# Kernel optimization log

Measured on AMD Instinct MI355X. Metric: run time of the kernel, lower is better.

## Reference

```python
import jax, jax.numpy as jnp
import numpy as np

H, HKV, D, HID = 64, 8, 64, 2880
T = 2048
WINDOW = 128
THETA = 150000.0
FACTOR = 32.0
ORIG_MAX = 4096
BETA_FAST, BETA_SLOW = 32.0, 1.0
EPS = 1e-5
SCALE = D ** -0.5
MSCALE = float(0.1 * np.log(FACTOR) + 1.0)  # vLLM YaRN attention mscale


def _yarn_inv_freq():
    # vLLM YaRNScalingRotaryEmbedding inverse frequencies
    def corr_dim(n_rot):
        return D * np.log(ORIG_MAX / (n_rot * 2.0 * np.pi)) / (2.0 * np.log(THETA))
    low = max(int(np.floor(corr_dim(BETA_FAST))), 0)
    high = min(int(np.ceil(corr_dim(BETA_SLOW))), D - 1)
    pow_ = np.arange(0, D, 2, dtype=np.float32) / D
    extrap = 1.0 / (THETA ** pow_)                 # extrapolation inv_freq
    interp = extrap / FACTOR                        # interpolation inv_freq
    ramp = np.clip((np.arange(D // 2, dtype=np.float32) - low) / max(high - low, 1e-3), 0.0, 1.0)
    extrap_mask = 1.0 - ramp
    inv_freq = interp * (1.0 - extrap_mask) + extrap * extrap_mask
    return jnp.asarray(inv_freq, jnp.float32)

_INV_FREQ = _yarn_inv_freq()


def _rope(positions, x):
    # neox-style rotation; x: [T, heads, D]
    freqs = positions.astype(jnp.float32)[:, None] * _INV_FREQ[None, :]  # [T, D/2]
    cos = (jnp.cos(freqs) * MSCALE)[:, None, :]
    sin = (jnp.sin(freqs) * MSCALE)[:, None, :]
    x1, x2 = x[..., : D // 2], x[..., D // 2 :]
    return jnp.concatenate([x1 * cos - x2 * sin, x2 * cos + x1 * sin], axis=-1)


def _attn(q, k, v, sinks):
    # q: [T,H,D]; k,v: [T,HKV,D]; sinks: [H] extra softmax logit per head
    g = H // HKV
    k = jnp.repeat(k, g, axis=1)
    v = jnp.repeat(v, g, axis=1)
    scores = jnp.einsum('qhd,khd->hqk', q, k) * SCALE  # [H,T,T]
    i = jnp.arange(T)[:, None]
    j = jnp.arange(T)[None, :]
    mask = (j <= i) & (i - j < WINDOW)  # causal + sliding window (even layer)
    scores = jnp.where(mask[None], scores, -jnp.inf)
    s = sinks[:, None]                                    # [H,1]
    m = jnp.maximum(jnp.max(scores, axis=-1), s)          # [H,T]
    p = jnp.exp(scores - m[..., None])                    # [H,T,T]
    denom = jnp.sum(p, axis=-1) + jnp.exp(s - m)          # sink adds to denominator only
    out = jnp.einsum('hqk,khd->qhd', p, v) / denom.T[..., None]
    return out.reshape(T, H * D)


def setup_inputs() -> dict:
    key = jax.random.key(0)
    ks = jax.random.split(key, 8)
    return {
        'hidden_states': jax.random.normal(ks[0], (T, HID), jnp.float32),
        'positions': jnp.arange(T, dtype=jnp.int32),
        'norm_w': jnp.ones((HID,), jnp.float32),
        'w_qkv': jax.random.normal(ks[1], ((H + 2 * HKV) * D, HID), jnp.float32) * 0.02,
        'b_qkv': jax.random.normal(ks[2], ((H + 2 * HKV) * D,), jnp.float32) * 0.02,
        'w_o': jax.random.normal(ks[3], (HID, H * D), jnp.float32) * 0.02,
        'b_o': jax.random.normal(ks[4], (HID,), jnp.float32) * 0.02,
        'sinks': jax.random.normal(ks[5], (H,), jnp.float32),
    }


def reference(hidden_states, positions, norm_w, w_qkv, b_qkv, w_o, b_o, sinks):
    x = hidden_states
    t = x * jax.lax.rsqrt(jnp.mean(x * x, axis=-1, keepdims=True) + EPS) * norm_w  # RMSNorm
    qkv = t @ w_qkv.T + b_qkv
    q, k, v = jnp.split(qkv, [H * D, H * D + HKV * D], axis=-1)
    q = _rope(positions, q.reshape(T, H, D))
    k = _rope(positions, k.reshape(T, HKV, D))
    v = v.reshape(T, HKV, D)
    attn_out = _attn(q, k, v, sinks)
    out = attn_out @ w_o.T + b_o
    return out + x  # residual
```

## Files before the change

### kernel.cpp

```cpp
#include <hip/hip_runtime.h>
#include <hip/hip_bf16.h>
#include <stdint.h>

typedef __attribute__((ext_vector_type(8))) short bf16x8;
typedef __attribute__((ext_vector_type(4))) float f32x4;
typedef __attribute__((ext_vector_type(4))) unsigned short u16x4;

#define T_SEQ 2048
#define HID_D 2880
#define KPAD 2944
#define NH 64
#define NKV 8
#define HD 64
#define QKV_N 5120
#define ATT_N 4096
#define WIN 128
#define RSCALE 0.125f
#define MSCALE 1.3465735903f
#define ROPE_TOT (T_SEQ * (NH + NKV) * 32)
#define VT_TOT (NKV * HD * T_SEQ)

__device__ __forceinline__ unsigned short f2bf(float f) {
  union { float f; unsigned u; } v; v.f = f;
  unsigned r = v.u + 0x7fffu + ((v.u >> 16) & 1u);
  return (unsigned short)(r >> 16);
}
__device__ __forceinline__ float bf2f(unsigned short u) {
  union { unsigned u; float f; } v; v.u = ((unsigned)u) << 16;
  return v.f;
}

__device__ __forceinline__ void gload_lds16(const void* g, void* l) {
  __builtin_amdgcn_global_load_lds((const __attribute__((address_space(1))) char*)g,
                                   (__attribute__((address_space(3))) char*)l, 16, 0, 0);
}

__global__ __launch_bounds__(256) void pre_kernel(const float* __restrict__ x,
                                                  const float* __restrict__ w,
                                                  unsigned short* __restrict__ t_bf,
                                                  const float* __restrict__ wq_src,
                                                  unsigned short* __restrict__ wq_dst) {
  __shared__ float red[256];
  if (blockIdx.x < 2048) {
    int row = blockIdx.x;
    const float4* xr4 = (const float4*)(x + (size_t)row * HID_D);
    const float4* w4 = (const float4*)w;
    float ss = 0.f;
    for (int i = threadIdx.x; i < 720; i += 256) {
      float4 v = xr4[i];
      ss += v.x * v.x + v.y * v.y + v.z * v.z + v.w * v.w;
    }
    red[threadIdx.x] = ss;
    __syncthreads();
    for (int s = 128; s > 0; s >>= 1) {
      if (threadIdx.x < s) red[threadIdx.x] += red[threadIdx.x + s];
      __syncthreads();
    }
    float rs = rsqrtf(red[0] / (float)HID_D + 1e-5f);
    u16x4* ob = (u16x4*)(t_bf + (size_t)row * KPAD);
    for (int i = threadIdx.x; i < 736; i += 256) {
      u16x4 o = {0, 0, 0, 0};
      if (i < 720) {
        float4 v = xr4[i];
        float4 g = w4[i];
        o = { f2bf(v.x * rs * g.x), f2bf(v.y * rs * g.y),
              f2bf(v.z * rs * g.z), f2bf(v.w * rs * g.w) };
      }
      ob[i] = o;
    }
  } else {
    const int total = QKV_N * 736;
    for (int i = (blockIdx.x - 2048) * 256 + threadIdx.x; i < total; i += 1024 * 256) {
      int c4 = i % 736, row = i / 736;
      u16x4 o = {0, 0, 0, 0};
      if (c4 < 720) {
        float4 v = ((const float4*)wq_src)[(size_t)row * 720 + c4];
        o = { f2bf(v.x), f2bf(v.y), f2bf(v.z), f2bf(v.w) };
      }
      ((u16x4*)wq_dst)[i] = o;
    }
  }
}

template <bool NCHECK, int MODE>
__device__ __forceinline__ void gemm_body(const unsigned short* __restrict__ A,
                                          const unsigned short* __restrict__ B,
                                          void* __restrict__ C0,
                                          float* __restrict__ Cpart,
                                          const float* __restrict__ bias,
                                          const float* __restrict__ resid,
                                          int M, int N, int ld, int nt,
                                          int nbx, int nbxy, int nstore, int swz,
                                          unsigned short* sA, unsigned short* sB) {
  const int tid = threadIdx.x;
  const int lane = tid & 63, wid = tid >> 6;
  const int wr = wid >> 2, wc = wid & 3;
  const int lq = lane & 15, ro = lane >> 4;

  const int kslice = swz / nbxy;
  const int rem = swz - kslice * nbxy;
  const int bx = rem % nbx, by = rem / nbx;
  const int m0 = by * 256, n0 = bx * 256;

  const unsigned short* Ab = A + (size_t)kslice * nt * 64;
  const unsigned short* Bb = B + (size_t)kslice * nt * 64;

  const int R0 = tid >> 3;
  const int g0 = (((tid & 7) ^ (R0 & 7)) << 3);
  const size_t aOff = (size_t)(m0 + R0) * ld + g0;
  size_t bOff[2][2];
#pragma unroll
  for (int h = 0; h < 2; ++h)
#pragma unroll
    for (int r = 0; r < 2; ++r) {
      int rr = n0 + h * 128 + r * 64 + R0;
      if (NCHECK) rr = min(rr, N - 1);
      bOff[h][r] = (size_t)rr * ld + g0;
    }

  const int ck0 = ((ro ^ (lq & 7)) << 3);
  const int ck1 = (((4 + ro) ^ (lq & 7)) << 3);

#define STG_A(BUF, H, KT)                                                        \
  { unsigned short* _d = sA + ((BUF) * 2 + (H)) * 8192 + wid * 512;              \
    const unsigned short* _s = Ab + aOff + (size_t)((H) * 128) * ld + (KT) * 64; \
    gload_lds16(_s, _d); gload_lds16(_s + (size_t)64 * ld, _d + 4096); }
#define STG_B(BUF, H, KT)                                                        \
  { unsigned short* _d = sB + ((BUF) * 2 + (H)) * 8192 + wid * 512;              \
    gload_lds16(Bb + bOff[H][0] + (KT) * 64, _d);                                \
    gload_lds16(Bb + bOff[H][1] + (KT) * 64, _d + 4096); }

  bf16x8 aR[8];
  bf16x8 bR0[4], bR1[4];
  f32x4 acc[8][4] = {};

#define LDA(BUF, S)                                                                        \
  { _Pragma("unroll") for (int ii = 0; ii < 4; ++ii) {                                     \
      const int _r = ((BUF) * 2 + wr) * 8192 + ((S) * 64 + ii * 16 + lq) * 64;             \
      aR[ii * 2 + 0] = *(const bf16x8*)&sA[_r + ck0];                                      \
      aR[ii * 2 + 1] = *(const bf16x8*)&sA[_r + ck1]; } }
#define LDB(BUF, NHF, DST)                                                                 \
  { _Pragma("unroll") for (int jj = 0; jj < 2; ++jj) {                                     \
      const int _r = ((BUF) * 2 + (wc >> 1)) * 8192 +                                      \
                     ((wc & 1) * 64 + ((NHF) * 2 + jj) * 16 + lq) * 64;                    \
      DST[jj * 2 + 0] = *(const bf16x8*)&sB[_r + ck0];                                     \
      DST[jj * 2 + 1] = *(const bf16x8*)&sB[_r + ck1]; } }
#define MFMA16(S, NHF, BREG)                                                               \
  { _Pragma("unroll") for (int ii = 0; ii < 4; ++ii)                                       \
    _Pragma("unroll") for (int jj = 0; jj < 2; ++jj)                                       \
    _Pragma("unroll") for (int kk = 0; kk < 2; ++kk)                                       \
      acc[(S) * 4 + ii][(NHF) * 2 + jj] = __builtin_amdgcn_mfma_f32_16x16x32_bf16(         \
          aR[ii * 2 + kk], BREG[jj * 2 + kk], acc[(S) * 4 + ii][(NHF) * 2 + jj], 0, 0, 0); }
#define PH_MID()                                         \
  __builtin_amdgcn_s_barrier();                          \
  asm volatile("s_waitcnt lgkmcnt(0)" ::: "memory");     \
  __builtin_amdgcn_sched_barrier(0);                     \
  __builtin_amdgcn_s_setprio(1)
#define PH_END()                                         \
  __builtin_amdgcn_s_setprio(0);                         \
  __builtin_amdgcn_s_barrier()

  STG_A(0, 0, 0); STG_A(0, 1, 0); STG_B(0, 0, 0); STG_B(0, 1, 0);
  STG_B(1, 0, 1); STG_B(1, 1, 1);
  asm volatile("s_waitcnt vmcnt(4)" ::: "memory");
  __builtin_amdgcn_s_barrier();

  const int niter = nt >> 1;
  for (int it = 0; it < niter; ++it) {
    const int t = it * 2;
    const bool more = (it + 1 < niter);
    LDA(0, 0); LDB(0, 0, bR0); STG_A(1, 0, t + 1);
    PH_MID(); MFMA16(0, 0, bR0); PH_END();
    LDB(0, 1, bR1); STG_A(1, 1, t + 1);
    PH_MID(); MFMA16(0, 1, bR1); PH_END();
    LDA(0, 1); if (more) STG_B(0, 0, t + 2);
    PH_MID(); MFMA16(1, 1, bR1); PH_END();
    if (more) STG_B(0, 1, t + 2);
    PH_MID(); MFMA16(1, 0, bR0);
    __builtin_amdgcn_s_setprio(0);
    if (more) asm volatile("s_waitcnt vmcnt(4)" ::: "memory");
    else      asm volatile("s_waitcnt vmcnt(0)" ::: "memory");
    __builtin_amdgcn_s_barrier();
    LDA(1, 0); LDB(1, 0, bR0); if (more) STG_A(0, 0, t + 2);
    PH_MID(); MFMA16(0, 0, bR0); PH_END();
    LDB(1, 1, bR1); if (more) STG_A(0, 1, t + 2);
    PH_MID(); MFMA16(0, 1, bR1); PH_END();
    LDA(1, 1); if (more) STG_B(1, 0, t + 3);
    PH_MID(); MFMA16(1, 1, bR1); PH_END();
    if (more) STG_B(1, 1, t + 3);
    PH_MID(); MFMA16(1, 0, bR0);
    __builtin_amdgcn_s_setprio(0);
    if (more) asm volatile("s_waitcnt vmcnt(4)" ::: "memory");
    else      asm volatile("s_waitcnt vmcnt(0)" ::: "memory");
    __builtin_amdgcn_s_barrier();
  }
#undef STG_A
#undef STG_B
#undef LDA
#undef LDB
#undef MFMA16
#undef PH_MID
#undef PH_END

#pragma unroll
  for (int fi = 0; fi < 8; ++fi) {
    const int gr = m0 + wr * 128 + fi * 16 + ro * 4;
#pragma unroll
    for (int j = 0; j < 4; ++j) {
      const int gc = n0 + wc * 64 + j * 16 + lq;
      if (!NCHECK || gc < N) {
        if (MODE == 2) {
          const float bv = bias[gc];
          unsigned short* Cs = (unsigned short*)C0;
#pragma unroll
          for (int r = 0; r < 4; ++r)
            Cs[(size_t)(gr + r) * nstore + gc] = f2bf(acc[fi][j][r] + bv);
        } else {
          if (kslice == 0) {
            float* Cf = (float*)C0;
            const float bv = bias[gc];
#pragma unroll
            for (int r = 0; r < 4; ++r) {
              size_t off = (size_t)(gr + r) * nstore + gc;
              Cf[off] = acc[fi][j][r] + bv + resid[off];
            }
          } else {
#pragma unroll
            for (int r = 0; r < 4; ++r)
              Cpart[(size_t)(gr + r) * nstore + gc] = acc[fi][j][r];
          }
        }
      }
    }
  }
}

__global__ __launch_bounds__(512, 2) void qkv_fused_kernel(const unsigned short* __restrict__ A,
                                                           const unsigned short* __restrict__ B,
                                                           unsigned short* __restrict__ C,
                                                           const float* __restrict__ bias,
                                                           const float* __restrict__ wo_src,
                                                           unsigned short* __restrict__ wo_dst) {
  __shared__ unsigned short sA[2 * 2 * 128 * 64];
  __shared__ unsigned short sB[2 * 2 * 128 * 64];
  const int c = blockIdx.x & 7, q = blockIdx.x >> 3;
  if (q < 20) {
    gemm_body<false, 2>(A, B, C, nullptr, bias, nullptr,
                        T_SEQ, QKV_N, KPAD, 46, 20, 160, QKV_N, c * 20 + q, sA, sB);
  } else {
    const int cid = c * 12 + (q - 20);
    const int total = HID_D * 1024;
    for (int i = cid * 512 + threadIdx.x; i < total; i += 96 * 512) {
      float4 v = ((const float4*)wo_src)[i];
      u16x4 o = { f2bf(v.x), f2bf(v.y), f2bf(v.z), f2bf(v.w) };
      ((u16x4*)wo_dst)[i] = o;
    }
  }
}

__global__ __launch_bounds__(512, 2) void outproj_kernel(const unsigned short* __restrict__ att,
                                                         const unsigned short* __restrict__ wo_bf,
                                                         float* __restrict__ out,
                                                         float* __restrict__ part,
                                                         const float* __restrict__ b_o,
                                                         const float* __restrict__ x) {
  __shared__ unsigned short sA[2 * 2 * 128 * 64];
  __shared__ unsigned short sB[2 * 2 * 128 * 64];
  const int swz = (blockIdx.x & 7) * 24 + (blockIdx.x >> 3);
  gemm_body<true, 1>(att, wo_bf, out, part, b_o, x,
                     T_SEQ, HID_D, ATT_N, 32, 12, 96, HID_D, swz, sA, sB);
}

__global__ __launch_bounds__(256) void reduce_add_kernel(float* __restrict__ out,
                                                         const float* __restrict__ part) {
  int i = blockIdx.x * 256 + threadIdx.x;
  if (i >= T_SEQ * 720) return;
  float4 o = ((const float4*)out)[i];
  float4 p = ((const float4*)part)[i];
  o.x += p.x; o.y += p.y; o.z += p.z; o.w += p.w;
  ((float4*)out)[i] = o;
}

__global__ __launch_bounds__(256) void ropev_kernel(const unsigned short* __restrict__ qkvb,
                                                    const int* __restrict__ positions,
                                                    unsigned short* __restrict__ qb,
                                                    unsigned short* __restrict__ kb,
                                                    unsigned short* __restrict__ vt) {
  int idx = blockIdx.x * 256 + threadIdx.x;
  if (idx < ROPE_TOT) {
    int d = idx & 31;
    int head = (idx >> 5) % (NH + NKV);
    int t = idx / ((NH + NKV) * 32);
    float pw = (float)d * (1.0f / 32.0f);
    float extrap = expf(-pw * 11.9183905733f);
    float interp = extrap * (1.0f / 32.0f);
    float ramp = fminf(fmaxf(((float)d - 8.0f) * 0.1f, 0.0f), 1.0f);
    float invf = interp * ramp + extrap * (1.0f - ramp);
    float fr = (float)positions[t] * invf;
    float s, c;
    sincosf(fr, &s, &c);
    c *= MSCALE;
    s *= MSCALE;
    if (head < NH) {
      const unsigned short* b = qkvb + (size_t)t * QKV_N + head * HD + d;
      float x1 = bf2f(b[0]), x2 = bf2f(b[32]);
      unsigned short* ob = qb + (size_t)t * ATT_N + head * HD + d;
      ob[0] = f2bf(x1 * c - x2 * s);
      ob[32] = f2bf(x2 * c + x1 * s);
    } else {
      int gk = head - NH;
      const unsigned short* b = qkvb + (size_t)t * QKV_N + NH * HD + gk * HD + d;
      float x1 = bf2f(b[0]), x2 = bf2f(b[32]);
      unsigned short* ob = kb + (size_t)t * (NKV * HD) + gk * HD + d;
      ob[0] = f2bf(x1 * c - x2 * s);
      ob[32] = f2bf(x2 * c + x1 * s);
    }
  } else {
    int i2 = idx - ROPE_TOT;
    int t = i2 & (T_SEQ - 1);
    int d = (i2 >> 11) & 63;
    int g = i2 >> 17;
    vt[i2] = qkvb[(size_t)t * QKV_N + (NH + NKV) * HD + g * HD + d];
  }
}

__global__ __launch_bounds__(256) void attn_kernel(const unsigned short* __restrict__ qb,
                                                   const unsigned short* __restrict__ kb,
                                                   const unsigned short* __restrict__ vt,
                                                   const float* __restrict__ sinks,
                                                   unsigned short* __restrict__ att) {
  const int lane = threadIdx.x & 63;
  const int wid = threadIdx.x >> 6;
  const int q0 = blockIdx.x * 16;
  const int h = blockIdx.y * 4 + wid;
  const int g = h >> 3;
  const int lq = lane & 15;
  const int ro = lane >> 4;

  bf16x8 bq0, bq1;
  {
    const unsigned short* qp = qb + (size_t)(q0 + lq) * ATT_N + h * HD + ro * 8;
    bq0 = *(const bf16x8*)qp;
    bq1 = *(const bf16x8*)(qp + 32);
  }
  float m_run = sinks[h];
  float l_run = 1.0f;
  f32x4 o0 = {0.f, 0.f, 0.f, 0.f}, o1 = o0, o2 = o0, o3 = o0;
  const int qg = q0 + lq;
  const int jstart = (q0 >= WIN) ? q0 - WIN : 0;

  for (int jt = jstart; jt <= q0; jt += 32) {
    f32x4 st0 = {0.f, 0.f, 0.f, 0.f}, st1 = st0;
    {
      int kr = jt + ((lq >> 2) << 3) + (lq & 3);
      int kr0 = min(kr, T_SEQ - 1);
      int kr1 = min(kr + 4, T_SEQ - 1);
      const unsigned short* kp0 = kb + (size_t)kr0 * (NKV * HD) + g * HD + ro * 8;
      const unsigned short* kp1 = kb + (size_t)kr1 * (NKV * HD) + g * HD + ro * 8;
      bf16x8 ka0a = *(const bf16x8*)kp0;
      bf16x8 ka0b = *(const bf16x8*)(kp0 + 32);
      bf16x8 ka1a = *(const bf16x8*)kp1;
      bf16x8 ka1b = *(const bf16x8*)(kp1 + 32);
      st0 = __builtin_amdgcn_mfma_f32_16x16x32_bf16(ka0a, bq0, st0, 0, 0, 0);
      st0 = __builtin_amdgcn_mfma_f32_16x16x32_bf16(ka0b, bq1, st0, 0, 0, 0);
      st1 = __builtin_amdgcn_mfma_f32_16x16x32_bf16(ka1a, bq0, st1, 0, 0, 0);
      st1 = __builtin_amdgcn_mfma_f32_16x16x32_bf16(ka1b, bq1, st1, 0, 0, 0);
    }
    float p[8];
    float tmax = -3.0e30f;
#pragma unroll
    for (int r = 0; r < 4; ++r) {
      int jg0 = jt + ro * 8 + r;
      int jg1 = jg0 + 4;
      float s0 = (jg0 <= qg && (qg - jg0) < WIN) ? st0[r] * RSCALE : -3.0e30f;
      float s1 = (jg1 <= qg && (qg - jg1) < WIN) ? st1[r] * RSCALE : -3.0e30f;
      p[r] = s0;
      p[r + 4] = s1;
      tmax = fmaxf(tmax, fmaxf(s0, s1));
    }
    tmax = fmaxf(tmax, __shfl_xor(tmax, 16));
    tmax = fmaxf(tmax, __shfl_xor(tmax, 32));
    float m_new = fmaxf(m_run, tmax);
    float rescale = expf(m_run - m_new);
    float psum = 0.f;
    bf16x8 pa;
#pragma unroll
    for (int jj = 0; jj < 8; ++jj) {
      float pe = expf(p[jj] - m_new);
      psum += pe;
      pa[jj] = (short)f2bf(pe);
    }
    psum += __shfl_xor(psum, 16);
    psum += __shfl_xor(psum, 32);
    l_run = l_run * rescale + psum;
    m_run = m_new;
    f32x4 rs4;
#pragma unroll
    for (int r = 0; r < 4; ++r) rs4[r] = __shfl(rescale, ro * 4 + r);
    o0 *= rs4; o1 *= rs4; o2 *= rs4; o3 *= rs4;
    int tb = jt + ro * 8;
    if (tb > T_SEQ - 8) tb = T_SEQ - 8;
    const unsigned short* vp = vt + (size_t)(g * HD + lq) * T_SEQ + tb;
    bf16x8 v0 = *(const bf16x8*)vp;
    bf16x8 v1 = *(const bf16x8*)(vp + 16 * T_SEQ);
    bf16x8 v2 = *(const bf16x8*)(vp + 32 * T_SEQ);
    bf16x8 v3 = *(const bf16x8*)(vp + 48 * T_SEQ);
    o0 = __builtin_amdgcn_mfma_f32_16x16x32_bf16(pa, v0, o0, 0, 0, 0);
    o1 = __builtin_amdgcn_mfma_f32_16x16x32_bf16(pa, v1, o1, 0, 0, 0);
    o2 = __builtin_amdgcn_mfma_f32_16x16x32_bf16(pa, v2, o2, 0, 0, 0);
    o3 = __builtin_amdgcn_mfma_f32_16x16x32_bf16(pa, v3, o3, 0, 0, 0);
  }

#pragma unroll
  for (int r = 0; r < 4; ++r) {
    float lr = __shfl(l_run, ro * 4 + r);
    float inv = 1.0f / lr;
    int qrow = q0 + ro * 4 + r;
    unsigned short* op = att + (size_t)qrow * ATT_N + h * HD + lq;
    op[0] = f2bf(o0[r] * inv);
    op[16] = f2bf(o1[r] * inv);
    op[32] = f2bf(o2[r] * inv);
    op[48] = f2bf(o3[r] * inv);
  }
}

extern "C" void kernel_launch(void* const* d_in, const int* in_sizes, int n_in,
                              void* d_out, int out_size, void* d_ws, size_t ws_size,
                              hipStream_t stream) {
  const float* x = (const float*)d_in[0];
  const int* pos = (const int*)d_in[1];
  const float* norm_w = (const float*)d_in[2];
  const float* w_qkv = (const float*)d_in[3];
  const float* b_qkv = (const float*)d_in[4];
  const float* w_o = (const float*)d_in[5];
  const float* b_o = (const float*)d_in[6];
  const float* sinks = (const float*)d_in[7];
  float* out = (float*)d_out;

  unsigned short* t_bf = (unsigned short*)d_ws;
  unsigned short* wq_bf = t_bf + (size_t)T_SEQ * KPAD;
  unsigned short* wo_bf = wq_bf + (size_t)QKV_N * KPAD;
  unsigned short* qkv_bf = wo_bf + (size_t)HID_D * ATT_N;
  unsigned short* qb = qkv_bf + (size_t)T_SEQ * QKV_N;
  unsigned short* kb = qb + (size_t)T_SEQ * ATT_N;
  unsigned short* vt = kb + (size_t)T_SEQ * NKV * HD;
  unsigned short* att = vt + (size_t)NKV * HD * T_SEQ;
  float* part = (float*)d_ws;

  pre_kernel<<<3072, 256, 0, stream>>>(x, norm_w, t_bf, w_qkv, wq_bf);
  qkv_fused_kernel<<<256, 512, 0, stream>>>(t_bf, wq_bf, qkv_bf, b_qkv, w_o, wo_bf);
  ropev_kernel<<<(ROPE_TOT + VT_TOT) / 256, 256, 0, stream>>>(qkv_bf, pos, qb, kb, vt);
  attn_kernel<<<dim3(T_SEQ / 16, NH / 4), 256, 0, stream>>>(qb, kb, vt, sinks, att);
  outproj_kernel<<<192, 512, 0, stream>>>(att, wo_bf, out, part, b_o, x);
  reduce_add_kernel<<<(T_SEQ * 720 + 255) / 256, 256, 0, stream>>>(out, part);
}
```

Baseline: 252.7 us.

## Fuse RoPE and V transpose into the QKV GEMM epilogue

Moves the YaRN rotary embedding for Q/K and the V transpose into the QKV GEMM epilogue. Each wave holds a full 64-wide head in its accumulators, so both rotation halves are available in registers. This removes the separate ropev kernel launch and the bf16 round trip of the QKV intermediate buffer through global memory. In exchange the epilogue now computes sincos per element inside the GEMM, which adds register pressure, and its stores are strided.

```diff
diff --git a/kernel.cpp b/kernel.cpp
--- a/kernel.cpp
+++ b/kernel.cpp
@@ -17,17 +17,19 @@
 #define WIN 128
 #define RSCALE 0.125f
 #define MSCALE 1.3465735903f
-#define ROPE_TOT (T_SEQ * (NH + NKV) * 32)
-#define VT_TOT (NKV * HD * T_SEQ)
 
 __device__ __forceinline__ unsigned short f2bf(float f) {
   union { float f; unsigned u; } v; v.f = f;
   unsigned r = v.u + 0x7fffu + ((v.u >> 16) & 1u);
   return (unsigned short)(r >> 16);
 }
-__device__ __forceinline__ float bf2f(unsigned short u) {
-  union { unsigned u; float f; } v; v.u = ((unsigned)u) << 16;
-  return v.f;
+
+__device__ __forceinline__ float yarn_invf(int dp) {
+  float pw = (float)dp * (1.0f / 32.0f);
+  float extrap = expf(-pw * 11.9183905733f);
+  float interp = extrap * (1.0f / 32.0f);
+  float ramp = fminf(fmaxf(((float)dp - 8.0f) * 0.1f, 0.0f), 1.0f);
+  return interp * ramp + extrap * (1.0f - ramp);
 }
 
 __device__ __forceinline__ void gload_lds16(const void* g, void* l) {
@@ -89,6 +91,10 @@
                                           float* __restrict__ Cpart,
                                           const float* __restrict__ bias,
                                           const float* __restrict__ resid,
+                                          unsigned short* __restrict__ qbp,
+                                          unsigned short* __restrict__ kbp,
+                                          unsigned short* __restrict__ vtp,
+                                          const int* __restrict__ positions,
                                           int M, int N, int ld, int nt,
                                           int nbx, int nbxy, int nstore, int swz,
                                           unsigned short* sA, unsigned short* sB) {
@@ -202,20 +208,63 @@
 #undef PH_MID
 #undef PH_END
 
-#pragma unroll
-  for (int fi = 0; fi < 8; ++fi) {
-    const int gr = m0 + wr * 128 + fi * 16 + ro * 4;
-#pragma unroll
-    for (int j = 0; j < 4; ++j) {
-      const int gc = n0 + wc * 64 + j * 16 + lq;
-      if (!NCHECK || gc < N) {
-        if (MODE == 2) {
-          const float bv = bias[gc];
-          unsigned short* Cs = (unsigned short*)C0;
-#pragma unroll
-          for (int r = 0; r < 4; ++r)
-            Cs[(size_t)(gr + r) * nstore + gc] = f2bf(acc[fi][j][r] + bv);
-        } else {
+  if (MODE == 3) {
+    const int cb = n0 + wc * 64;
+    const int hh = cb >> 6;
+    const float bv0 = bias[cb + lq];
+    const float bv1 = bias[cb + 16 + lq];
+    const float bv2 = bias[cb + 32 + lq];
+    const float bv3 = bias[cb + 48 + lq];
+    if (hh < NH + NKV) {
+      const float invf0 = yarn_invf(lq);
+      const float invf1 = yarn_invf(16 + lq);
+      unsigned short* dst;
+      int stride;
+      if (hh < NH) { dst = qbp + hh * HD; stride = ATT_N; }
+      else         { dst = kbp + (hh - NH) * HD; stride = NKV * HD; }
+#pragma unroll
+      for (int fi = 0; fi < 8; ++fi) {
+        const int gr = m0 + wr * 128 + fi * 16 + ro * 4;
+#pragma unroll
+        for (int r = 0; r < 4; ++r) {
+          const int t = gr + r;
+          const float pos = (float)positions[t];
+          float s0, c0, s1, c1;
+          sincosf(pos * invf0, &s0, &c0);
+          sincosf(pos * invf1, &s1, &c1);
+          c0 *= MSCALE; s0 *= MSCALE; c1 *= MSCALE; s1 *= MSCALE;
+          const float x1a = acc[fi][0][r] + bv0, x2a = acc[fi][2][r] + bv2;
+          const float x1b = acc[fi][1][r] + bv1, x2b = acc[fi][3][r] + bv3;
+          unsigned short* p = dst + (size_t)t * stride;
+          p[lq]      = f2bf(x1a * c0 - x2a * s0);
+          p[lq + 32] = f2bf(x2a * c0 + x1a * s0);
+          p[lq + 16] = f2bf(x1b * c1 - x2b * s1);
+          p[lq + 48] = f2bf(x2b * c1 + x1b * s1);
+        }
+      }
+    } else {
+      const int g = hh - (NH + NKV);
+      const float bvs[4] = {bv0, bv1, bv2, bv3};
+#pragma unroll
+      for (int fi = 0; fi < 8; ++fi) {
+        const int gr = m0 + wr * 128 + fi * 16 + ro * 4;
+#pragma unroll
+        for (int j = 0; j < 4; ++j) {
+          const int d = j * 16 + lq;
+          ushort4 w = { f2bf(acc[fi][j][0] + bvs[j]), f2bf(acc[fi][j][1] + bvs[j]),
+                        f2bf(acc[fi][j][2] + bvs[j]), f2bf(acc[fi][j][3] + bvs[j]) };
+          *(ushort4*)(vtp + (size_t)(g * HD + d) * T_SEQ + gr) = w;
+        }
+      }
+    }
+  } else {
+#pragma unroll
+    for (int fi = 0; fi < 8; ++fi) {
+      const int gr = m0 + wr * 128 + fi * 16 + ro * 4;
+#pragma unroll
+      for (int j = 0; j < 4; ++j) {
+        const int gc = n0 + wc * 64 + j * 16 + lq;
+        if (!NCHECK || gc < N) {
           if (kslice == 0) {
             float* Cf = (float*)C0;
             const float bv = bias[gc];
@@ -237,15 +286,18 @@
 
 __global__ __launch_bounds__(512, 2) void qkv_fused_kernel(const unsigned short* __restrict__ A,
                                                            const unsigned short* __restrict__ B,
-                                                           unsigned short* __restrict__ C,
                                                            const float* __restrict__ bias,
+                                                           unsigned short* __restrict__ qb,
+                                                           unsigned short* __restrict__ kb,
+                                                           unsigned short* __restrict__ vt,
+                                                           const int* __restrict__ positions,
                                                            const float* __restrict__ wo_src,
                                                            unsigned short* __restrict__ wo_dst) {
   __shared__ unsigned short sA[2 * 2 * 128 * 64];
   __shared__ unsigned short sB[2 * 2 * 128 * 64];
   const int c = blockIdx.x & 7, q = blockIdx.x >> 3;
   if (q < 20) {
-    gemm_body<false, 2>(A, B, C, nullptr, bias, nullptr,
+    gemm_body<false, 3>(A, B, nullptr, nullptr, bias, nullptr, qb, kb, vt, positions,
                         T_SEQ, QKV_N, KPAD, 46, 20, 160, QKV_N, c * 20 + q, sA, sB);
   } else {
     const int cid = c * 12 + (q - 20);
@@ -267,7 +319,7 @@
   __shared__ unsigned short sA[2 * 2 * 128 * 64];
   __shared__ unsigned short sB[2 * 2 * 128 * 64];
   const int swz = (blockIdx.x & 7) * 24 + (blockIdx.x >> 3);
-  gemm_body<true, 1>(att, wo_bf, out, part, b_o, x,
+  gemm_body<true, 1>(att, wo_bf, out, part, b_o, x, nullptr, nullptr, nullptr, nullptr,
                      T_SEQ, HID_D, ATT_N, 32, 12, 96, HID_D, swz, sA, sB);
 }
 
@@ -279,49 +331,6 @@
   float4 p = ((const float4*)part)[i];
   o.x += p.x; o.y += p.y; o.z += p.z; o.w += p.w;
   ((float4*)out)[i] = o;
-}
-
-__global__ __launch_bounds__(256) void ropev_kernel(const unsigned short* __restrict__ qkvb,
-                                                    const int* __restrict__ positions,
-                                                    unsigned short* __restrict__ qb,
-                                                    unsigned short* __restrict__ kb,
-                                                    unsigned short* __restrict__ vt) {
-  int idx = blockIdx.x * 256 + threadIdx.x;
-  if (idx < ROPE_TOT) {
-    int d = idx & 31;
-    int head = (idx >> 5) % (NH + NKV);
-    int t = idx / ((NH + NKV) * 32);
-    float pw = (float)d * (1.0f / 32.0f);
-    float extrap = expf(-pw * 11.9183905733f);
-    float interp = extrap * (1.0f / 32.0f);
-    float ramp = fminf(fmaxf(((float)d - 8.0f) * 0.1f, 0.0f), 1.0f);
-    float invf = interp * ramp + extrap * (1.0f - ramp);
-    float fr = (float)positions[t] * invf;
-    float s, c;
-    sincosf(fr, &s, &c);
-    c *= MSCALE;
-    s *= MSCALE;
-    if (head < NH) {
-      const unsigned short* b = qkvb + (size_t)t * QKV_N + head * HD + d;
-      float x1 = bf2f(b[0]), x2 = bf2f(b[32]);
-      unsigned short* ob = qb + (size_t)t * ATT_N + head * HD + d;
-      ob[0] = f2bf(x1 * c - x2 * s);
-      ob[32] = f2bf(x2 * c + x1 * s);
-    } else {
-      int gk = head - NH;
-      const unsigned short* b = qkvb + (size_t)t * QKV_N + NH * HD + gk * HD + d;
-      float x1 = bf2f(b[0]), x2 = bf2f(b[32]);
-      unsigned short* ob = kb + (size_t)t * (NKV * HD) + gk * HD + d;
-      ob[0] = f2bf(x1 * c - x2 * s);
-      ob[32] = f2bf(x2 * c + x1 * s);
-    }
-  } else {
-    int i2 = idx - ROPE_TOT;
-    int t = i2 & (T_SEQ - 1);
-    int d = (i2 >> 11) & 63;
-    int g = i2 >> 17;
-    vt[i2] = qkvb[(size_t)t * QKV_N + (NH + NKV) * HD + g * HD + d];
-  }
 }
 
 __global__ __launch_bounds__(256) void attn_kernel(const unsigned short* __restrict__ qb,
@@ -440,16 +449,14 @@
   unsigned short* t_bf = (unsigned short*)d_ws;
   unsigned short* wq_bf = t_bf + (size_t)T_SEQ * KPAD;
   unsigned short* wo_bf = wq_bf + (size_t)QKV_N * KPAD;
-  unsigned short* qkv_bf = wo_bf + (size_t)HID_D * ATT_N;
-  unsigned short* qb = qkv_bf + (size_t)T_SEQ * QKV_N;
+  unsigned short* qb = wo_bf + (size_t)HID_D * ATT_N;
   unsigned short* kb = qb + (size_t)T_SEQ * ATT_N;
   unsigned short* vt = kb + (size_t)T_SEQ * NKV * HD;
   unsigned short* att = vt + (size_t)NKV * HD * T_SEQ;
   float* part = (float*)d_ws;
 
   pre_kernel<<<3072, 256, 0, stream>>>(x, norm_w, t_bf, w_qkv, wq_bf);
-  qkv_fused_kernel<<<256, 512, 0, stream>>>(t_bf, wq_bf, qkv_bf, b_qkv, w_o, wo_bf);
-  ropev_kernel<<<(ROPE_TOT + VT_TOT) / 256, 256, 0, stream>>>(qkv_bf, pos, qb, kb, vt);
+  qkv_fused_kernel<<<256, 512, 0, stream>>>(t_bf, wq_bf, b_qkv, qb, kb, vt, pos, w_o, wo_bf);
   attn_kernel<<<dim3(T_SEQ / 16, NH / 4), 256, 0, stream>>>(qb, kb, vt, sinks, att);
   outproj_kernel<<<192, 512, 0, stream>>>(att, wo_bf, out, part, b_o, x);
   reduce_add_kernel<<<(T_SEQ * 720 + 255) / 256, 256, 0, stream>>>(out, part);
```

Measured after the change: 277.0 us. +9.6%, slower.

## Replace split-K partial buffer and reduce kernel with atomic accumulation into output

Applied to the files above, without the earlier changes.

The output is pre-initialised with residual plus bias in the idle blocks of the QKV GEMM kernel. The two-slice split-K out-projection then atomically adds its accumulators into the output, so the separate reduce_add kernel and the partial buffer's write and read-back go away. In exchange it uses fp32 atomics, roughly 5.9M per slice, and the summation order is no longer fixed. It also relies on the output initialisation finishing before the out-projection runs.

```diff
diff --git a/kernel.cpp b/kernel.cpp
--- a/kernel.cpp
+++ b/kernel.cpp
@@ -86,9 +86,7 @@
 __device__ __forceinline__ void gemm_body(const unsigned short* __restrict__ A,
                                           const unsigned short* __restrict__ B,
                                           void* __restrict__ C0,
-                                          float* __restrict__ Cpart,
                                           const float* __restrict__ bias,
-                                          const float* __restrict__ resid,
                                           int M, int N, int ld, int nt,
                                           int nbx, int nbxy, int nstore, int swz,
                                           unsigned short* sA, unsigned short* sB) {
@@ -216,19 +214,10 @@
           for (int r = 0; r < 4; ++r)
             Cs[(size_t)(gr + r) * nstore + gc] = f2bf(acc[fi][j][r] + bv);
         } else {
-          if (kslice == 0) {
-            float* Cf = (float*)C0;
-            const float bv = bias[gc];
-#pragma unroll
-            for (int r = 0; r < 4; ++r) {
-              size_t off = (size_t)(gr + r) * nstore + gc;
-              Cf[off] = acc[fi][j][r] + bv + resid[off];
-            }
-          } else {
-#pragma unroll
-            for (int r = 0; r < 4; ++r)
-              Cpart[(size_t)(gr + r) * nstore + gc] = acc[fi][j][r];
-          }
+          float* Cf = (float*)C0;
+#pragma unroll
+          for (int r = 0; r < 4; ++r)
+            atomicAdd(&Cf[(size_t)(gr + r) * nstore + gc], acc[fi][j][r]);
         }
       }
     }
@@ -240,12 +229,15 @@
                                                            unsigned short* __restrict__ C,
                                                            const float* __restrict__ bias,
                                                            const float* __restrict__ wo_src,
-                                                           unsigned short* __restrict__ wo_dst) {
+                                                           unsigned short* __restrict__ wo_dst,
+                                                           const float* __restrict__ x,
+                                                           const float* __restrict__ b_o,
+                                                           float* __restrict__ out) {
   __shared__ unsigned short sA[2 * 2 * 128 * 64];
   __shared__ unsigned short sB[2 * 2 * 128 * 64];
   const int c = blockIdx.x & 7, q = blockIdx.x >> 3;
   if (q < 20) {
-    gemm_body<false, 2>(A, B, C, nullptr, bias, nullptr,
+    gemm_body<false, 2>(A, B, C, bias,
                         T_SEQ, QKV_N, KPAD, 46, 20, 160, QKV_N, c * 20 + q, sA, sB);
   } else {
     const int cid = c * 12 + (q - 20);
@@ -255,30 +247,25 @@
       u16x4 o = { f2bf(v.x), f2bf(v.y), f2bf(v.z), f2bf(v.w) };
       ((u16x4*)wo_dst)[i] = o;
     }
+    const int tot2 = T_SEQ * 720;
+    for (int i = cid * 512 + threadIdx.x; i < tot2; i += 96 * 512) {
+      int c4 = i % 720;
+      float4 xv = ((const float4*)x)[i];
+      float4 bv = ((const float4*)b_o)[c4];
+      float4 o = { xv.x + bv.x, xv.y + bv.y, xv.z + bv.z, xv.w + bv.w };
+      ((float4*)out)[i] = o;
+    }
   }
 }
 
 __global__ __launch_bounds__(512, 2) void outproj_kernel(const unsigned short* __restrict__ att,
                                                          const unsigned short* __restrict__ wo_bf,
-                                                         float* __restrict__ out,
-                                                         float* __restrict__ part,
-                                                         const float* __restrict__ b_o,
-                                                         const float* __restrict__ x) {
+                                                         float* __restrict__ out) {
   __shared__ unsigned short sA[2 * 2 * 128 * 64];
   __shared__ unsigned short sB[2 * 2 * 128 * 64];
   const int swz = (blockIdx.x & 7) * 24 + (blockIdx.x >> 3);
-  gemm_body<true, 1>(att, wo_bf, out, part, b_o, x,
+  gemm_body<true, 1>(att, wo_bf, out, nullptr,
                      T_SEQ, HID_D, ATT_N, 32, 12, 96, HID_D, swz, sA, sB);
-}
-
-__global__ __launch_bounds__(256) void reduce_add_kernel(float* __restrict__ out,
-                                                         const float* __restrict__ part) {
-  int i = blockIdx.x * 256 + threadIdx.x;
-  if (i >= T_SEQ * 720) return;
-  float4 o = ((const float4*)out)[i];
-  float4 p = ((const float4*)part)[i];
-  o.x += p.x; o.y += p.y; o.z += p.z; o.w += p.w;
-  ((float4*)out)[i] = o;
 }
 
 __global__ __launch_bounds__(256) void ropev_kernel(const unsigned short* __restrict__ qkvb,
@@ -445,12 +432,11 @@
   unsigned short* kb = qb + (size_t)T_SEQ * ATT_N;
   unsigned short* vt = kb + (size_t)T_SEQ * NKV * HD;
   unsigned short* att = vt + (size_t)NKV * HD * T_SEQ;
-  float* part = (float*)d_ws;
 
   pre_kernel<<<3072, 256, 0, stream>>>(x, norm_w, t_bf, w_qkv, wq_bf);
-  qkv_fused_kernel<<<256, 512, 0, stream>>>(t_bf, wq_bf, qkv_bf, b_qkv, w_o, wo_bf);
+  qkv_fused_kernel<<<256, 512, 0, stream>>>(t_bf, wq_bf, qkv_bf, b_qkv, w_o, wo_bf,
+                                            x, b_o, out);
   ropev_kernel<<<(ROPE_TOT + VT_TOT) / 256, 256, 0, stream>>>(qkv_bf, pos, qb, kb, vt);
   attn_kernel<<<dim3(T_SEQ / 16, NH / 4), 256, 0, stream>>>(qb, kb, vt, sinks, att);
-  outproj_kernel<<<192, 512, 0, stream>>>(att, wo_bf, out, part, b_o, x);
-  reduce_add_kernel<<<(T_SEQ * 720 + 255) / 256, 256, 0, stream>>>(out, part);
-}
+  outproj_kernel<<<192, 512, 0, stream>>>(att, wo_bf, out);
+}
```

New measurement: 255.5 us. About the same (+1.1%).

## Replace split-K out-projection with 128-row tile GEMM and drop reduce kernel

Applied to the files above, without the earlier changes.

The out-projection GEMM no longer uses split-K (two K slices plus a separate reduce_add pass over a float partial buffer). It now uses a dedicated kernel with 128x256 tiles over the full K, 192 blocks, a triple-buffered B stage and double-buffered A, and writes bias plus residual directly. This removes the partial-sum write/read traffic and one kernel launch. The QKV GEMM block mapping is also remapped so each XCD gets a contiguous 4x5 tile region for L2 locality. The trade-off is a longer K loop per block and a different LDS footprint.

```diff
diff --git a/kernel.cpp b/kernel.cpp
--- a/kernel.cpp
+++ b/kernel.cpp
@@ -82,28 +82,20 @@
   }
 }
 
-template <bool NCHECK, int MODE>
 __device__ __forceinline__ void gemm_body(const unsigned short* __restrict__ A,
                                           const unsigned short* __restrict__ B,
-                                          void* __restrict__ C0,
-                                          float* __restrict__ Cpart,
+                                          unsigned short* __restrict__ C,
                                           const float* __restrict__ bias,
-                                          const float* __restrict__ resid,
-                                          int M, int N, int ld, int nt,
-                                          int nbx, int nbxy, int nstore, int swz,
+                                          int N, int ld, int nt,
+                                          int nbx, int nstore, int swz,
                                           unsigned short* sA, unsigned short* sB) {
   const int tid = threadIdx.x;
   const int lane = tid & 63, wid = tid >> 6;
   const int wr = wid >> 2, wc = wid & 3;
   const int lq = lane & 15, ro = lane >> 4;
 
-  const int kslice = swz / nbxy;
-  const int rem = swz - kslice * nbxy;
-  const int bx = rem % nbx, by = rem / nbx;
+  const int bx = swz % nbx, by = swz / nbx;
   const int m0 = by * 256, n0 = bx * 256;
-
-  const unsigned short* Ab = A + (size_t)kslice * nt * 64;
-  const unsigned short* Bb = B + (size_t)kslice * nt * 64;
 
   const int R0 = tid >> 3;
   const int g0 = (((tid & 7) ^ (R0 & 7)) << 3);
@@ -114,7 +106,6 @@
 #pragma unroll
     for (int r = 0; r < 2; ++r) {
       int rr = n0 + h * 128 + r * 64 + R0;
-      if (NCHECK) rr = min(rr, N - 1);
       bOff[h][r] = (size_t)rr * ld + g0;
     }
 
@@ -123,12 +114,12 @@
 
 #define STG_A(BUF, H, KT)                                                        \
   { unsigned short* _d = sA + ((BUF) * 2 + (H)) * 8192 + wid * 512;              \
-    const unsigned short* _s = Ab + aOff + (size_t)((H) * 128) * ld + (KT) * 64; \
+    const unsigned short* _s = A + aOff + (size_t)((H) * 128) * ld + (KT) * 64;  \
     gload_lds16(_s, _d); gload_lds16(_s + (size_t)64 * ld, _d + 4096); }
 #define STG_B(BUF, H, KT)                                                        \
   { unsigned short* _d = sB + ((BUF) * 2 + (H)) * 8192 + wid * 512;              \
-    gload_lds16(Bb + bOff[H][0] + (KT) * 64, _d);                                \
-    gload_lds16(Bb + bOff[H][1] + (KT) * 64, _d + 4096); }
+    gload_lds16(B + bOff[H][0] + (KT) * 64, _d);                                 \
+    gload_lds16(B + bOff[H][1] + (KT) * 64, _d + 4096); }
 
   bf16x8 aR[8];
   bf16x8 bR0[4], bR1[4];
@@ -208,29 +199,10 @@
 #pragma unroll
     for (int j = 0; j < 4; ++j) {
       const int gc = n0 + wc * 64 + j * 16 + lq;
-      if (!NCHECK || gc < N) {
-        if (MODE == 2) {
-          const float bv = bias[gc];
-          unsigned short* Cs = (unsigned short*)C0;
-#pragma unroll
-          for (int r = 0; r < 4; ++r)
-            Cs[(size_t)(gr + r) * nstore + gc] = f2bf(acc[fi][j][r] + bv);
-        } else {
-          if (kslice == 0) {
-            float* Cf = (float*)C0;
-            const float bv = bias[gc];
-#pragma unroll
-            for (int r = 0; r < 4; ++r) {
-              size_t off = (size_t)(gr + r) * nstore + gc;
-              Cf[off] = acc[fi][j][r] + bv + resid[off];
-            }
-          } else {
-#pragma unroll
-            for (int r = 0; r < 4; ++r)
-              Cpart[(size_t)(gr + r) * nstore + gc] = acc[fi][j][r];
-          }
-        }
-      }
+      const float bv = bias[gc];
+#pragma unroll
+      for (int r = 0; r < 4; ++r)
+        C[(size_t)(gr + r) * nstore + gc] = f2bf(acc[fi][j][r] + bv);
     }
   }
 }
@@ -245,8 +217,9 @@
   __shared__ unsigned short sB[2 * 2 * 128 * 64];
   const int c = blockIdx.x & 7, q = blockIdx.x >> 3;
   if (q < 20) {
-    gemm_body<false, 2>(A, B, C, nullptr, bias, nullptr,
-                        T_SEQ, QKV_N, KPAD, 46, 20, 160, QKV_N, c * 20 + q, sA, sB);
+    const int by = (c & 1) * 4 + (q & 3);
+    const int bx = (c >> 1) * 5 + (q >> 2);
+    gemm_body(A, B, C, bias, QKV_N, KPAD, 46, 20, QKV_N, by * 20 + bx, sA, sB);
   } else {
     const int cid = c * 12 + (q - 20);
     const int total = HID_D * 1024;
@@ -258,27 +231,134 @@
   }
 }
 
-__global__ __launch_bounds__(512, 2) void outproj_kernel(const unsigned short* __restrict__ att,
-                                                         const unsigned short* __restrict__ wo_bf,
-                                                         float* __restrict__ out,
-                                                         float* __restrict__ part,
-                                                         const float* __restrict__ b_o,
-                                                         const float* __restrict__ x) {
-  __shared__ unsigned short sA[2 * 2 * 128 * 64];
-  __shared__ unsigned short sB[2 * 2 * 128 * 64];
-  const int swz = (blockIdx.x & 7) * 24 + (blockIdx.x >> 3);
-  gemm_body<true, 1>(att, wo_bf, out, part, b_o, x,
-                     T_SEQ, HID_D, ATT_N, 32, 12, 96, HID_D, swz, sA, sB);
-}
-
-__global__ __launch_bounds__(256) void reduce_add_kernel(float* __restrict__ out,
-                                                         const float* __restrict__ part) {
-  int i = blockIdx.x * 256 + threadIdx.x;
-  if (i >= T_SEQ * 720) return;
-  float4 o = ((const float4*)out)[i];
-  float4 p = ((const float4*)part)[i];
-  o.x += p.x; o.y += p.y; o.z += p.z; o.w += p.w;
-  ((float4*)out)[i] = o;
+__global__ __launch_bounds__(512, 2) void outproj128_kernel(const unsigned short* __restrict__ att,
+                                                            const unsigned short* __restrict__ wo,
+                                                            float* __restrict__ out,
+                                                            const float* __restrict__ b_o,
+                                                            const float* __restrict__ x) {
+  __shared__ unsigned short sA[2 * 128 * 64];
+  __shared__ unsigned short sB[3 * 2 * 128 * 64];
+
+  const int tid = threadIdx.x;
+  const int lane = tid & 63, wid = tid >> 6;
+  const int wr = wid >> 2, wc = wid & 3;
+  const int lq = lane & 15, ro = lane >> 4;
+
+  const int c = blockIdx.x & 7, q = blockIdx.x >> 3;
+  const int by = (c & 1) * 8 + (q & 7);
+  const int bx = (c >> 1) * 3 + (q >> 3);
+  const int m0 = by * 128, n0 = bx * 256;
+
+  const int R0 = tid >> 3;
+  const int g0 = (((tid & 7) ^ (R0 & 7)) << 3);
+  const size_t aOff = (size_t)(m0 + R0) * ATT_N + g0;
+  size_t bOff[2][2];
+#pragma unroll
+  for (int h = 0; h < 2; ++h)
+#pragma unroll
+    for (int r = 0; r < 2; ++r) {
+      int rr = min(n0 + h * 128 + r * 64 + R0, HID_D - 1);
+      bOff[h][r] = (size_t)rr * ATT_N + g0;
+    }
+
+  const int ck0 = ((ro ^ (lq & 7)) << 3);
+  const int ck1 = (((4 + ro) ^ (lq & 7)) << 3);
+
+#define OSTG_A(BUF, KT)                                                         \
+  { unsigned short* _d = sA + (BUF) * 8192 + wid * 512;                         \
+    const unsigned short* _s = att + aOff + (size_t)(KT) * 64;                  \
+    gload_lds16(_s, _d); gload_lds16(_s + (size_t)64 * ATT_N, _d + 4096); }
+#define OSTG_B(BUF, H, KT)                                                      \
+  { unsigned short* _d = sB + ((BUF) * 2 + (H)) * 8192 + wid * 512;             \
+    gload_lds16(wo + bOff[H][0] + (KT) * 64, _d);                               \
+    gload_lds16(wo + bOff[H][1] + (KT) * 64, _d + 4096); }
+
+  bf16x8 aR[8];
+  bf16x8 bR0[4], bR1[4];
+  f32x4 acc[4][4] = {};
+
+#define OLDA(BUF)                                                                          \
+  { _Pragma("unroll") for (int ii = 0; ii < 4; ++ii) {                                     \
+      const int _r = (BUF) * 8192 + (wr * 64 + ii * 16 + lq) * 64;                         \
+      aR[ii * 2 + 0] = *(const bf16x8*)&sA[_r + ck0];                                      \
+      aR[ii * 2 + 1] = *(const bf16x8*)&sA[_r + ck1]; } }
+#define OLDB(BUF, NHF, DST)                                                                \
+  { _Pragma("unroll") for (int jj = 0; jj < 2; ++jj) {                                     \
+      const int _r = ((BUF) * 2 + (wc >> 1)) * 8192 +                                      \
+                     ((wc & 1) * 64 + ((NHF) * 2 + jj) * 16 + lq) * 64;                    \
+      DST[jj * 2 + 0] = *(const bf16x8*)&sB[_r + ck0];                                     \
+      DST[jj * 2 + 1] = *(const bf16x8*)&sB[_r + ck1]; } }
+#define OMFMA(NHF, BREG)                                                                   \
+  { _Pragma("unroll") for (int ii = 0; ii < 4; ++ii)                                       \
+    _Pragma("unroll") for (int jj = 0; jj < 2; ++jj)                                       \
+    _Pragma("unroll") for (int kk = 0; kk < 2; ++kk)                                       \
+      acc[ii][(NHF) * 2 + jj] = __builtin_amdgcn_mfma_f32_16x16x32_bf16(                   \
+          aR[ii * 2 + kk], BREG[jj * 2 + kk], acc[ii][(NHF) * 2 + jj], 0, 0, 0); }
+#define OPH_MID()                                        \
+  __builtin_amdgcn_s_barrier();                          \
+  asm volatile("s_waitcnt lgkmcnt(0)" ::: "memory");     \
+  __builtin_amdgcn_sched_barrier(0);                     \
+  __builtin_amdgcn_s_setprio(1)
+#define OPH_END()                                        \
+  __builtin_amdgcn_s_setprio(0);                         \
+  __builtin_amdgcn_s_barrier()
+
+  OSTG_B(0, 0, 0); OSTG_B(0, 1, 0); OSTG_A(0, 0);
+  OSTG_B(1, 0, 1); OSTG_B(1, 1, 1); OSTG_A(1, 1);
+  asm volatile("s_waitcnt vmcnt(6)" ::: "memory");
+  __builtin_amdgcn_s_barrier();
+
+  const int nt = 64;
+  for (int it = 0; it < nt / 2; ++it) {
+    const int T = it * 2;
+    const bool more = (T + 2 < nt);
+    const int bb0 = T % 3, bb1 = (T + 1) % 3;
+    const int bb2 = (T + 2) % 3, bb3 = (T + 3) % 3;
+    OLDA(T & 1); OLDB(bb0, 0, bR0);
+    if (more) { OSTG_B(bb2, 0, T + 2); OSTG_B(bb2, 1, T + 2); }
+    OPH_MID(); OMFMA(0, bR0); OPH_END();
+    OLDB(bb0, 1, bR1);
+    if (more) OSTG_A(T & 1, T + 2);
+    OPH_MID(); OMFMA(1, bR1);
+    __builtin_amdgcn_s_setprio(0);
+    if (more) asm volatile("s_waitcnt vmcnt(6)" ::: "memory");
+    else      asm volatile("s_waitcnt vmcnt(0)" ::: "memory");
+    __builtin_amdgcn_s_barrier();
+    OLDA((T + 1) & 1); OLDB(bb1, 0, bR0);
+    if (more) { OSTG_B(bb3, 0, T + 3); OSTG_B(bb3, 1, T + 3); }
+    OPH_MID(); OMFMA(0, bR0); OPH_END();
+    OLDB(bb1, 1, bR1);
+    if (more) OSTG_A((T + 1) & 1, T + 3);
+    OPH_MID(); OMFMA(1, bR1);
+    __builtin_amdgcn_s_setprio(0);
+    if (more) asm volatile("s_waitcnt vmcnt(6)" ::: "memory");
+    else      asm volatile("s_waitcnt vmcnt(0)" ::: "memory");
+    __builtin_amdgcn_s_barrier();
+  }
+#undef OSTG_A
+#undef OSTG_B
+#undef OLDA
+#undef OLDB
+#undef OMFMA
+#undef OPH_MID
+#undef OPH_END
+
+#pragma unroll
+  for (int ii = 0; ii < 4; ++ii) {
+    const int gr = m0 + wr * 64 + ii * 16 + ro * 4;
+#pragma unroll
+    for (int j = 0; j < 4; ++j) {
+      const int gc = n0 + wc * 64 + j * 16 + lq;
+      if (gc < HID_D) {
+        const float bv = b_o[gc];
+#pragma unroll
+        for (int r = 0; r < 4; ++r) {
+          size_t off = (size_t)(gr + r) * HID_D + gc;
+          out[off] = acc[ii][j][r] + bv + x[off];
+        }
+      }
+    }
+  }
 }
 
 __global__ __launch_bounds__(256) void ropev_kernel(const unsigned short* __restrict__ qkvb,
@@ -445,12 +525,10 @@
   unsigned short* kb = qb + (size_t)T_SEQ * ATT_N;
   unsigned short* vt = kb + (size_t)T_SEQ * NKV * HD;
   unsigned short* att = vt + (size_t)NKV * HD * T_SEQ;
-  float* part = (float*)d_ws;
 
   pre_kernel<<<3072, 256, 0, stream>>>(x, norm_w, t_bf, w_qkv, wq_bf);
   qkv_fused_kernel<<<256, 512, 0, stream>>>(t_bf, wq_bf, qkv_bf, b_qkv, w_o, wo_bf);
   ropev_kernel<<<(ROPE_TOT + VT_TOT) / 256, 256, 0, stream>>>(qkv_bf, pos, qb, kb, vt);
   attn_kernel<<<dim3(T_SEQ / 16, NH / 4), 256, 0, stream>>>(qb, kb, vt, sinks, att);
-  outproj_kernel<<<192, 512, 0, stream>>>(att, wo_bf, out, part, b_o, x);
-  reduce_add_kernel<<<(T_SEQ * 720 + 255) / 256, 256, 0, stream>>>(out, part);
-}
+  outproj128_kernel<<<192, 512, 0, stream>>>(att, wo_bf, out, b_o, x);
+}
```

New measurement: 249.9 us. No clear change (-1.1%).
